# Kernel tuning notes

Measured on AMD Instinct MI355X. Metric: run time of the kernel, lower is better.

Reference implementation:

```python
import jax, jax.numpy as jnp
import numpy as np

NUM_GROUPS = 50
ALPHA = 2.0  # epoch=1, alpha_step=50 -> alpha never incremented


def setup_inputs() -> dict:
    key = jax.random.key(0)
    k1, k2, k3, k4 = jax.random.split(key, 4)
    B, C, N = 2, 64, 8192
    l0_points = jax.random.normal(k1, (B, C, N), dtype=jnp.float32)
    W = jax.random.normal(k2, (3, C), dtype=jnp.float32) * 0.1  # conv2_1 1x1 kernel
    b = jax.random.normal(k3, (3,), dtype=jnp.float32) * 0.1
    target = jax.random.randint(k4, (B, N), 0, NUM_GROUPS, dtype=jnp.int64)
    return {"l0_points": l0_points, "W": W, "b": b, "target": target}


def reference(l0_points, W, b, target):
    # Fsim = conv2_1(l0_points) : 1x1 conv == channel matmul. [B, 3, N]
    Fsim = jnp.einsum("oc,bcn->bon", W, l0_points) + b[None, :, None]
    # pairwise squared euclidean distance matrix D[b,i,j] = ||f_i - f_j||^2
    r = jnp.sum(Fsim * Fsim, axis=1)  # [B, N]
    mul = 2.0 * jnp.einsum("bcn,bcm->bnm", Fsim, Fsim)  # [B, N, N]
    D = r[:, None, :] - mul + r[:, :, None]
    D = jnp.maximum(D, 0.0)  # D[D <= 0] = 0
    # group one-hot (labels == -1 masked out)
    valid = (target != -1)[..., None].astype(D.dtype)
    one_hot = jax.nn.one_hot(target, NUM_GROUPS, dtype=D.dtype) * valid  # [B, N, G]
    same = jnp.einsum("bng,bmg->bnm", one_hot, one_hot)  # [B, N, N]
    N = same.shape[1]
    eye = jnp.eye(N, dtype=bool)
    same = jnp.where(eye[None, :, :], 1.0, same)  # diag forced to 1
    diff = 1.0 - same
    inv_sq = 1.0 / ((D + 1.0) * (D + 1.0))
    simmat_loss = 100.0 * (ALPHA * diff * inv_sq + same * D)
    return jnp.mean(simmat_loss)
```

## Files before the change

### kernel.cpp

```cpp
#include <hip/hip_runtime.h>

#define NPTS    8192
#define BATCH   2
#define CH      64
#define NGROUPS 50

#define TS      256
#define NROW    32
#define NTILEB  (NROW*(NROW+1)/2)
#define MAINPB  (NTILEB*2)
#define MAINB   (BATCH*MAINPB)
#define NBUCK   (BATCH*NGROUPS)
#define CORRB   (NBUCK*4)
#define PAD     256

__global__ __launch_bounds__(256) void fsim_kernel(
    const float* __restrict__ l0, const float* __restrict__ W,
    const float* __restrict__ bias, const int* __restrict__ target,
    float4* __restrict__ fj4, int* __restrict__ gidx, int* __restrict__ gcnt)
{
    const int bid = blockIdx.x, tid = threadIdx.x;

    if (bid < 256) {
        __shared__ float sW[3 * CH];
        if (tid < 3 * CH) sW[tid] = W[tid];
        __syncthreads();
        const int lane = tid & 63, wave = tid >> 6;
        const int p = lane & 15, cg = lane >> 4;
        const int pt = bid * 64 + wave * 16 + p;
        const int b = pt >> 13, n = pt & (NPTS - 1);
        const float* basep = l0 + (size_t)b * CH * NPTS + n;
        float ax = 0.f, ay = 0.f, az = 0.f;
        #pragma unroll
        for (int k = 0; k < 16; ++k) {
            int c = cg * 16 + k;
            float v = basep[(size_t)c * NPTS];
            ax = fmaf(sW[c], v, ax);
            ay = fmaf(sW[CH + c], v, ay);
            az = fmaf(sW[2*CH + c], v, az);
        }
        ax += __shfl_down(ax,32,64); ay += __shfl_down(ay,32,64); az += __shfl_down(az,32,64);
        ax += __shfl_down(ax,16,64); ay += __shfl_down(ay,16,64); az += __shfl_down(az,16,64);
        if (cg == 0) {
            float X = ax + bias[0], Y = ay + bias[1], Z = az + bias[2];
            fj4[pt] = make_float4(X, Y, Z, fmaf(X, X, fmaf(Y, Y, Z * Z)));
        }
    } else {
        const int bucket = bid - 256;
        const int b = bucket / NGROUPS, L = bucket % NGROUPS;
        const int tbase = b * NPTS;
        __shared__ int scnt[256];
        int cnt = 0;
        const int4* t4 = (const int4*)&target[tbase];
        #pragma unroll
        for (int k8 = 0; k8 < 8; ++k8) {
            int4 tv = t4[tid * 8 + k8];
            cnt += (tv.x == L) + (tv.y == L) + (tv.z == L) + (tv.w == L);
        }
        scnt[tid] = cnt;
        __syncthreads();
        for (int s = 1; s < 256; s <<= 1) {
            int a = (tid >= s) ? scnt[tid - s] : 0;
            __syncthreads();
            scnt[tid] += a;
            __syncthreads();
        }
        int wpos = scnt[tid] - cnt;
        for (int k = 0; k < 32; ++k) {
            int idx = tid * 32 + k;
            if (target[tbase + idx] == L) {
                if (wpos < PAD) gidx[bucket * PAD + wpos] = idx;
                ++wpos;
            }
        }
        if (tid == 0) gcnt[bucket] = min(scnt[255], PAD);
    }
}

__global__ __launch_bounds__(256) void pair_kernel(
    const float4* __restrict__ fj4,
    const int* __restrict__ gidx, const int* __restrict__ gcnt,
    double* __restrict__ partials)
{
    const int bid = blockIdx.x, tid = threadIdx.x;
    __shared__ float4 sj[PAD];
    __shared__ double wsum[4];

    float  accv = 0.0f;
    double cadd = 0.0;

    if (bid < CORRB) {
        const int bucket = bid >> 2, sub = bid & 3;
        const int b = bucket / NGROUPS;
        const int cnt = gcnt[bucket];
        const int base = b * NPTS;
        {
            float4 pv = make_float4(0.f, 0.f, 0.f, 0.f);
            if (tid < cnt) {
                float4 g = fj4[base + gidx[bucket * PAD + tid]];
                pv = make_float4(g.x, g.y, g.z, 1.0f);
            }
            sj[tid] = pv;
        }
        __syncthreads();
        const int pp = sub * 64 + (tid & 63);
        const int g0 = (tid >> 6) * 64;
        if (pp < cnt) {
            const float4 a = sj[pp];
            float accB = 0.f;
            #pragma unroll 4
            for (int qq = g0; qq < g0 + 64; ++qq) {
                float4 c = sj[qq];
                float dx = a.x - c.x, dy = a.y - c.y, dz = a.z - c.z;
                float t = fmaf(dx, dx, fmaf(dy, dy, fmaf(dz, dz, 1.0f)));
                float rr = __builtin_amdgcn_rcpf(t); rr = rr * rr;
                accB = fmaf(fmaf(-2.0f, rr, t), c.w, accB);
            }
            accv = accB;
        }
        if (sub == 0 && tid == 0) {
            double c = (double)cnt;
            cadd = 2.0 * c - c * c;
        }
        __syncthreads();
    }

    {
        const int b   = bid / MAINPB;
        const int r   = bid % MAINPB;
        const int tau = r >> 1, half = r & 1;
        int ti = (int)(32.5f - sqrtf(32.5f * 32.5f - 2.0f * (float)tau));
        if (ti < 0) ti = 0; if (ti > NROW - 1) ti = NROW - 1;
        while ((ti + 1) * (65 - (ti + 1)) / 2 <= tau) ++ti;
        while (ti * (65 - ti) / 2 > tau) --ti;
        const int tj = ti + (tau - ti * (65 - ti) / 2);

        const int base = b * NPTS;
        const int ib = base + ti * TS + (tid & 63) * 4;
        const float4 p0 = fj4[ib + 0], p1 = fj4[ib + 1];
        const float4 p2 = fj4[ib + 2], p3 = fj4[ib + 3];
        const float nx[4] = {-2.f*p0.x, -2.f*p1.x, -2.f*p2.x, -2.f*p3.x};
        const float ny[4] = {-2.f*p0.y, -2.f*p1.y, -2.f*p2.y, -2.f*p3.y};
        const float nz[4] = {-2.f*p0.z, -2.f*p1.z, -2.f*p2.z, -2.f*p3.z};
        const float si[4] = {p0.w+1.f, p1.w+1.f, p2.w+1.f, p3.w+1.f};

        const int jb = __builtin_amdgcn_readfirstlane(
                           base + tj * TS + half * 128 + (tid >> 6) * 32);

        float acc[4] = {0.f, 0.f, 0.f, 0.f};
        #pragma unroll 8
        for (int jj = 0; jj < 32; ++jj) {
            const float4 q = fj4[jb + jj];
            #pragma unroll
            for (int u = 0; u < 4; ++u) {
                float t = si[u] + q.w;
                t = fmaf(nx[u], q.x, t);
                t = fmaf(ny[u], q.y, t);
                t = fmaf(nz[u], q.z, t);
                float rcp = __builtin_amdgcn_rcpf(t);
                acc[u] = fmaf(rcp, rcp, acc[u]);
            }
        }
        float s = (acc[0] + acc[1]) + (acc[2] + acc[3]);
        accv += (ti == tj) ? (2.0f * s) : (4.0f * s);
    }

    #pragma unroll
    for (int o = 32; o > 0; o >>= 1) accv += __shfl_down(accv, o, 64);
    if ((tid & 63) == 0) wsum[tid >> 6] = (double)accv;
    __syncthreads();
    if (tid == 0)
        partials[bid] = (wsum[0] + wsum[1]) + (wsum[2] + wsum[3]) + cadd;
}

__global__ __launch_bounds__(256) void finalize_kernel(
    const double* __restrict__ partials, float* __restrict__ out)
{
    const int tid = threadIdx.x;
    double s = 0.0;
    for (int k = tid; k < MAINB; k += 256) s += partials[k];
    #pragma unroll
    for (int o = 32; o > 0; o >>= 1) s += __shfl_down(s, o, 64);
    __shared__ double sd[4];
    if ((tid & 63) == 0) sd[tid >> 6] = s;
    __syncthreads();
    if (tid == 0) {
        double tot = (sd[0] + sd[1]) + (sd[2] + sd[3]);
        tot -= 2.0 * (double)(BATCH * NPTS);
        out[0] = (float)(100.0 * tot / ((double)BATCH * NPTS * NPTS));
    }
}

extern "C" void kernel_launch(void* const* d_in, const int* in_sizes, int n_in,
                              void* d_out, int out_size, void* d_ws, size_t ws_size,
                              hipStream_t stream) {
    const float* l0     = (const float*)d_in[0];
    const float* W      = (const float*)d_in[1];
    const float* bias   = (const float*)d_in[2];
    const int*   target = (const int*)d_in[3];
    float* out = (float*)d_out;

    float4* fj4      = (float4*)d_ws;
    double* partials = (double*)((char*)d_ws + BATCH * NPTS * sizeof(float4));
    int*    gidx     = (int*)((char*)partials + MAINB * sizeof(double));
    int*    gcnt     = gidx + NBUCK * PAD;

    fsim_kernel<<<256 + NBUCK, 256, 0, stream>>>(l0, W, bias, target, fj4, gidx, gcnt);
    pair_kernel<<<MAINB, 256, 0, stream>>>(fj4, gidx, gcnt, partials);
    finalize_kernel<<<1, 256, 0, stream>>>(partials, out);
}
```

Baseline: 34.27 us.

## Split correction and main pair work into separate blocks, drop block-level reduction

The correction work on same-group pairs no longer shares blocks with the main tile work. Those blocks now run in their own part of a larger grid (CORRB + MAINB blocks), so correction blocks no longer delay main tiles. The per-block shared-memory reduction and its syncthreads are removed: each wave writes its own partial, and the finalize kernel sums four times as many partials. The readfirstlane hint on the j pointer is also dropped, which may turn scalar loads into vector loads.

```diff
diff --git a/kernel.cpp b/kernel.cpp
--- a/kernel.cpp
+++ b/kernel.cpp
@@ -6,12 +6,13 @@
 #define NGROUPS 50
 
 #define TS      256
-#define NROW    32
+#define NROW    (NPTS/TS)
 #define NTILEB  (NROW*(NROW+1)/2)
 #define MAINPB  (NTILEB*2)
 #define MAINB   (BATCH*MAINPB)
 #define NBUCK   (BATCH*NGROUPS)
 #define CORRB   (NBUCK*4)
+#define GRID_T  (CORRB+MAINB)
 #define PAD     256
 
 __global__ __launch_bounds__(256) void fsim_kernel(
@@ -83,13 +84,51 @@
     double* __restrict__ partials)
 {
     const int bid = blockIdx.x, tid = threadIdx.x;
-    __shared__ float4 sj[PAD];
-    __shared__ double wsum[4];
+    const int lane = tid & 63, wave = tid >> 6;
 
     float  accv = 0.0f;
     double cadd = 0.0;
 
-    if (bid < CORRB) {
+    if (bid >= CORRB) {
+        const int mid = bid - CORRB;
+        const int b   = mid / MAINPB;
+        const int r   = mid % MAINPB;
+        const int tau = r >> 1, half = r & 1;
+        int ti = (int)(32.5f - sqrtf(32.5f * 32.5f - 2.0f * (float)tau));
+        if (ti < 0) ti = 0; if (ti > NROW - 1) ti = NROW - 1;
+        while ((ti + 1) * (65 - (ti + 1)) / 2 <= tau) ++ti;
+        while (ti * (65 - ti) / 2 > tau) --ti;
+        const int tj = ti + (tau - ti * (65 - ti) / 2);
+
+        const int base = b * NPTS;
+        const int ib = base + ti * TS + lane * 4;
+        const float4 p0 = fj4[ib + 0], p1 = fj4[ib + 1];
+        const float4 p2 = fj4[ib + 2], p3 = fj4[ib + 3];
+        const float nx[4] = {-2.f*p0.x, -2.f*p1.x, -2.f*p2.x, -2.f*p3.x};
+        const float ny[4] = {-2.f*p0.y, -2.f*p1.y, -2.f*p2.y, -2.f*p3.y};
+        const float nz[4] = {-2.f*p0.z, -2.f*p1.z, -2.f*p2.z, -2.f*p3.z};
+        const float si[4] = {p0.w+1.f, p1.w+1.f, p2.w+1.f, p3.w+1.f};
+
+        const float4* jp = &fj4[base + tj * TS + half * 128 + wave * 32];
+
+        float acc[4] = {0.f, 0.f, 0.f, 0.f};
+        #pragma unroll 8
+        for (int jj = 0; jj < 32; ++jj) {
+            const float4 q = jp[jj];
+            #pragma unroll
+            for (int u = 0; u < 4; ++u) {
+                float t = si[u] + q.w;
+                t = fmaf(nx[u], q.x, t);
+                t = fmaf(ny[u], q.y, t);
+                t = fmaf(nz[u], q.z, t);
+                float rcp = __builtin_amdgcn_rcpf(t);
+                acc[u] = fmaf(rcp, rcp, acc[u]);
+            }
+        }
+        float s = (acc[0] + acc[1]) + (acc[2] + acc[3]);
+        accv = (ti == tj) ? (2.0f * s) : (4.0f * s);
+    } else {
+        __shared__ float4 sj[PAD];
         const int bucket = bid >> 2, sub = bid & 3;
         const int b = bucket / NGROUPS;
         const int cnt = gcnt[bucket];
@@ -103,8 +142,8 @@
             sj[tid] = pv;
         }
         __syncthreads();
-        const int pp = sub * 64 + (tid & 63);
-        const int g0 = (tid >> 6) * 64;
+        const int pp = sub * 64 + lane;
+        const int g0 = wave * 64;
         if (pp < cnt) {
             const float4 a = sj[pp];
             float accB = 0.f;
@@ -118,59 +157,16 @@
             }
             accv = accB;
         }
-        if (sub == 0 && tid == 0) {
+        if (sub == 0 && wave == 0 && lane == 0) {
             double c = (double)cnt;
             cadd = 2.0 * c - c * c;
         }
-        __syncthreads();
-    }
-
-    {
-        const int b   = bid / MAINPB;
-        const int r   = bid % MAINPB;
-        const int tau = r >> 1, half = r & 1;
-        int ti = (int)(32.5f - sqrtf(32.5f * 32.5f - 2.0f * (float)tau));
-        if (ti < 0) ti = 0; if (ti > NROW - 1) ti = NROW - 1;
-        while ((ti + 1) * (65 - (ti + 1)) / 2 <= tau) ++ti;
-        while (ti * (65 - ti) / 2 > tau) --ti;
-        const int tj = ti + (tau - ti * (65 - ti) / 2);
-
-        const int base = b * NPTS;
-        const int ib = base + ti * TS + (tid & 63) * 4;
-        const float4 p0 = fj4[ib + 0], p1 = fj4[ib + 1];
-        const float4 p2 = fj4[ib + 2], p3 = fj4[ib + 3];
-        const float nx[4] = {-2.f*p0.x, -2.f*p1.x, -2.f*p2.x, -2.f*p3.x};
-        const float ny[4] = {-2.f*p0.y, -2.f*p1.y, -2.f*p2.y, -2.f*p3.y};
-        const float nz[4] = {-2.f*p0.z, -2.f*p1.z, -2.f*p2.z, -2.f*p3.z};
-        const float si[4] = {p0.w+1.f, p1.w+1.f, p2.w+1.f, p3.w+1.f};
-
-        const int jb = __builtin_amdgcn_readfirstlane(
-                           base + tj * TS + half * 128 + (tid >> 6) * 32);
-
-        float acc[4] = {0.f, 0.f, 0.f, 0.f};
-        #pragma unroll 8
-        for (int jj = 0; jj < 32; ++jj) {
-            const float4 q = fj4[jb + jj];
-            #pragma unroll
-            for (int u = 0; u < 4; ++u) {
-                float t = si[u] + q.w;
-                t = fmaf(nx[u], q.x, t);
-                t = fmaf(ny[u], q.y, t);
-                t = fmaf(nz[u], q.z, t);
-                float rcp = __builtin_amdgcn_rcpf(t);
-                acc[u] = fmaf(rcp, rcp, acc[u]);
-            }
-        }
-        float s = (acc[0] + acc[1]) + (acc[2] + acc[3]);
-        accv += (ti == tj) ? (2.0f * s) : (4.0f * s);
     }
 
     #pragma unroll
     for (int o = 32; o > 0; o >>= 1) accv += __shfl_down(accv, o, 64);
-    if ((tid & 63) == 0) wsum[tid >> 6] = (double)accv;
-    __syncthreads();
-    if (tid == 0)
-        partials[bid] = (wsum[0] + wsum[1]) + (wsum[2] + wsum[3]) + cadd;
+    if (lane == 0)
+        partials[bid * 4 + wave] = (double)accv + cadd;
 }
 
 __global__ __launch_bounds__(256) void finalize_kernel(
@@ -178,7 +174,7 @@
 {
     const int tid = threadIdx.x;
     double s = 0.0;
-    for (int k = tid; k < MAINB; k += 256) s += partials[k];
+    for (int k = tid; k < GRID_T * 4; k += 256) s += partials[k];
     #pragma unroll
     for (int o = 32; o > 0; o >>= 1) s += __shfl_down(s, o, 64);
     __shared__ double sd[4];
@@ -202,10 +198,10 @@
 
     float4* fj4      = (float4*)d_ws;
     double* partials = (double*)((char*)d_ws + BATCH * NPTS * sizeof(float4));
-    int*    gidx     = (int*)((char*)partials + MAINB * sizeof(double));
+    int*    gidx     = (int*)((char*)partials + GRID_T * 4 * sizeof(double));
     int*    gcnt     = gidx + NBUCK * PAD;
 
     fsim_kernel<<<256 + NBUCK, 256, 0, stream>>>(l0, W, bias, target, fj4, gidx, gcnt);
-    pair_kernel<<<MAINB, 256, 0, stream>>>(fj4, gidx, gcnt, partials);
+    pair_kernel<<<GRID_T, 256, 0, stream>>>(fj4, gidx, gcnt, partials);
     finalize_kernel<<<1, 256, 0, stream>>>(partials, out);
 }
```

New measurement: 42.37 us. +23.7%, slower.
